# Optimization experiments

Hardware: AMD Instinct MI355X
Metric: run time of the kernel (lower is better)

## Reference

```python
import jax, jax.numpy as jnp
import numpy as np

B, L, D, H = 4, 2048, 512, 8
HD = D // H
NEG = -1e9


def setup_inputs() -> dict:
    key = jax.random.key(0)
    ks = jax.random.split(key, 11)
    s = 1.0 / np.sqrt(D)
    inp = {
        "q": jax.random.normal(ks[0], (B, L, D), jnp.float32),
        "k": jax.random.normal(ks[1], (B, L, D), jnp.float32),
        "v": jax.random.normal(ks[2], (B, L, D), jnp.float32),
        "mask": jnp.broadcast_to(jnp.tril(jnp.ones((L, L), jnp.int32)), (B, L, L)),
        "Wq": jax.random.normal(ks[3], (D, D), jnp.float32) * s,
        "bq": jax.random.normal(ks[4], (D,), jnp.float32) * s,
        "Wk": jax.random.normal(ks[5], (D, D), jnp.float32) * s,
        "bk": jax.random.normal(ks[6], (D,), jnp.float32) * s,
        "Wv": jax.random.normal(ks[7], (D, D), jnp.float32) * s,
        "bv": jax.random.normal(ks[8], (D,), jnp.float32) * s,
        "Wo": jax.random.normal(ks[9], (D, D), jnp.float32) * s,
        "bo": jax.random.normal(ks[10], (D,), jnp.float32) * s,
    }
    return inp


def reference(q, k, v, mask, Wq, bq, Wk, bk, Wv, bv, Wo, bo):
    # Linear projections (torch Linear: x @ W.T + b)
    Q = (q @ Wq.T + bq).reshape(B, L, H, HD).transpose(0, 2, 1, 3)  # [B,H,L,hd]
    K = (k @ Wk.T + bk).reshape(B, L, H, HD).transpose(0, 2, 1, 3)
    V = (v @ Wv.T + bv).reshape(B, L, H, HD).transpose(0, 2, 1, 3)
    # scaled dot-product attention with masked_fill(mask==0, -1e9)
    score = jnp.einsum('bhqd,bhkd->bhqk', Q, K) / jnp.sqrt(jnp.float32(HD))
    score = jnp.where(mask[:, None, :, :] == 0, NEG, score)
    attn = jax.nn.softmax(score, axis=-1)
    ctx = jnp.einsum('bhqk,bhkd->bhqd', attn, V)  # [B,H,L,hd]
    ctx = ctx.transpose(0, 2, 1, 3).reshape(B, L, D)
    return ctx @ Wo.T + bo
```

## Files before the change

### kernel.cpp

```cpp
#include <hip/hip_runtime.h>
#include <hip/hip_bf16.h>
#include <math.h>

constexpr int Bc  = 4;
constexpr int Lc  = 2048;
constexpr int Dc  = 512;
constexpr int Hc  = 8;
constexpr int HDc = 64;

constexpr int GK = Dc;
constexpr int BK = 64;

typedef __attribute__((ext_vector_type(8))) short bf16x8;
typedef __attribute__((ext_vector_type(4))) short bf16x4;
typedef __attribute__((ext_vector_type(4))) float f32x4;
typedef __attribute__((ext_vector_type(16))) float f32x16;
typedef __attribute__((ext_vector_type(4))) int i32x4;

static __device__ __forceinline__ short f2bf(float x) {
    __hip_bfloat16 h = __float2bfloat16(x);
    return (short)__builtin_bit_cast(unsigned short, h);
}

static __device__ __forceinline__ int cvtpk_bf16(float lo, float hi) {
    int r;
    asm("v_cvt_pk_bf16_f32 %0, %1, %2" : "=v"(r) : "v"(lo), "v"(hi));
    return r;
}

static __device__ __forceinline__ void gload_lds16(const void* g, void* l) {
    __builtin_amdgcn_global_load_lds(
        (const __attribute__((address_space(1))) void*)g,
        (__attribute__((address_space(3))) void*)l, 16, 0, 0);
}

__global__ __launch_bounds__(256)
void cast_all(const float* __restrict__ q, const float* __restrict__ k,
              const float* __restrict__ v, const float* __restrict__ wq,
              const float* __restrict__ wk, const float* __restrict__ wv,
              const float* __restrict__ wo, short* __restrict__ dst) {
    const size_t i = ((size_t)blockIdx.x * 256 + threadIdx.x) * 8;
    const float* src; size_t off;
    if      (i <  4194304) { src = q;  off = i; }
    else if (i <  8388608) { src = k;  off = i -  4194304; }
    else if (i < 12582912) { src = v;  off = i -  8388608; }
    else if (i < 12845056) { src = wq; off = i - 12582912; }
    else if (i < 13107200) { src = wk; off = i - 12845056; }
    else if (i < 13369344) { src = wv; off = i - 13107200; }
    else                   { src = wo; off = i - 13369344; }
    const float4 a = *(const float4*)(src + off);
    const float4 b = *(const float4*)(src + off + 4);
    bf16x8 o;
    o[0] = f2bf(a.x); o[1] = f2bf(a.y); o[2] = f2bf(a.z); o[3] = f2bf(a.w);
    o[4] = f2bf(b.x); o[5] = f2bf(b.y); o[6] = f2bf(b.z); o[7] = f2bf(b.w);
    *(bf16x8*)(dst + i) = o;
}

template<int BM, int BN, int WMT, int WNT>
__device__ __forceinline__ void gemm_tile(const short* __restrict__ A,
                                          const short* __restrict__ W,
                                          short* As, short* Bs,
                                          f32x4 (&acc)[WMT][WNT],
                                          int m0, int n0) {
    const int tid  = threadIdx.x;
    const int w    = tid >> 6;
    const int lane = tid & 63;
    const int low4 = lane & 15;
    const int quad = lane >> 4;
    const int wm   = w & 1, wn = w >> 1;
    const int lrow = lane >> 3;
    const int lchk = (lane & 7) * 8;

    for (int k0 = 0; k0 < GK; k0 += BK) {
#pragma unroll
        for (int i = 0; i < BM / 32; ++i) {
            const int r0 = i * 32 + w * 8;
            gload_lds16(A + (size_t)(m0 + r0 + lrow) * GK + k0 + lchk, As + r0 * BK);
        }
#pragma unroll
        for (int i = 0; i < BN / 32; ++i) {
            const int r0 = i * 32 + w * 8;
            gload_lds16(W + (size_t)(n0 + r0 + lrow) * GK + k0 + lchk, Bs + r0 * BK);
        }
        __syncthreads();
#pragma unroll
        for (int ks = 0; ks < 2; ++ks) {
            bf16x8 af[WMT], bfr[WNT];
#pragma unroll
            for (int mi = 0; mi < WMT; ++mi)
                af[mi] = *(const bf16x8*)(As + (wm * WMT * 16 + mi * 16 + low4) * BK + ks * 32 + quad * 8);
#pragma unroll
            for (int ni = 0; ni < WNT; ++ni)
                bfr[ni] = *(const bf16x8*)(Bs + (wn * WNT * 16 + ni * 16 + low4) * BK + ks * 32 + quad * 8);
#pragma unroll
            for (int mi = 0; mi < WMT; ++mi)
#pragma unroll
                for (int ni = 0; ni < WNT; ++ni)
                    acc[mi][ni] = __builtin_amdgcn_mfma_f32_16x16x32_bf16(af[mi], bfr[ni], acc[mi][ni], 0, 0, 0);
        }
        __syncthreads();
    }
}

__global__ __launch_bounds__(256)
void qkv_gemm(const short* __restrict__ Xq, const short* __restrict__ Xk,
              const short* __restrict__ Xv, const short* __restrict__ Wcat,
              const float* __restrict__ bq, const float* __restrict__ bk,
              const float* __restrict__ bv,
              short* __restrict__ Qw, short* __restrict__ Kw, short* __restrict__ Vw) {
    __shared__ __align__(16) short Smem[128 * 138];
    short* As = Smem;
    short* Bs = Smem + 8192;
    short* Ts = Smem;

    const int tid = threadIdx.x;
    const int i    = blockIdx.x;
    const int slot = i >> 3;
    const int g    = (i & 7) + 8 * (slot >> 2);
    const int j    = slot & 3;
    const int z    = g >> 6;
    const int m0   = (g & 63) * 128;
    const int n0   = z * 512 + j * 128;

    const short* A    = (z == 0) ? Xq : (z == 1) ? Xk : Xv;
    const float* bias = (z == 0) ? bq : (z == 1) ? bk : bv;

    f32x4 acc[4][4];
#pragma unroll
    for (int mi = 0; mi < 4; ++mi)
#pragma unroll
        for (int ni = 0; ni < 4; ++ni) acc[mi][ni] = (f32x4){0.f, 0.f, 0.f, 0.f};

    gemm_tile<128, 128, 4, 4>(A, Wcat, As, Bs, acc, m0, n0);

    const int lane = tid & 63, w = tid >> 6;
    const int low4 = lane & 15, quad = lane >> 4;
    const int wm = w & 1, wn = w >> 1;

    if (z < 2) {
        short* Y = (z == 0) ? Qw : Kw;
#pragma unroll
        for (int mi = 0; mi < 4; ++mi)
#pragma unroll
            for (int ni = 0; ni < 4; ++ni)
#pragma unroll
                for (int r = 0; r < 4; ++r) {
                    const int rowL = wm * 64 + mi * 16 + quad * 4 + r;
                    const int colL = wn * 64 + ni * 16 + low4;
                    const int c    = (n0 & 511) + colL;
                    Ts[rowL * 138 + colL] = f2bf(acc[mi][ni][r] + bias[c]);
                }
        __syncthreads();
        const int jj = tid & 7;
        const int b = m0 >> 11;
#pragma unroll
        for (int it = 0; it < 8; ++it) {
            const int slot2 = it * 32 + (tid >> 3);
            const int row  = slot2 >> 1, half = slot2 & 1;
            const int c0 = (n0 & 511) + half * 64;
            const int h  = c0 >> 6;
            const int l  = (m0 & 2047) + row;
            short* dst = Y + (((size_t)b * Hc + h) * Lc + l) * HDc + jj * 8;
            *(bf16x8*)dst = *(const bf16x8*)(Ts + row * 138 + half * 64 + jj * 8);
        }
    } else {
#pragma unroll
        for (int mi = 0; mi < 4; ++mi)
#pragma unroll
            for (int ni = 0; ni < 4; ++ni)
#pragma unroll
                for (int r = 0; r < 4; ++r) {
                    const int rowL = wm * 64 + mi * 16 + quad * 4 + r;
                    const int colL = wn * 64 + ni * 16 + low4;
                    const int c    = (n0 + colL) & 511;
                    Ts[colL * 136 + rowL] = f2bf(acc[mi][ni][r] + bias[c]);
                }
        __syncthreads();
        const int hdl = tid >> 1, seg = tid & 1;
        const int c  = (n0 + hdl) & 511;
        const int h  = c >> 6, hd = c & 63;
        const int b  = m0 >> 11, l0 = (m0 & 2047) + seg * 64;
        short* dst = Vw + (((size_t)b * Hc + h) * HDc + hd) * Lc + l0;
        const short* srcT = Ts + hdl * 136 + seg * 64;
#pragma unroll
        for (int jj = 0; jj < 8; ++jj)
            *(bf16x8*)(dst + jj * 8) = *(const bf16x8*)(srcT + jj * 8);
    }
}

__global__ __launch_bounds__(256)
void out_gemm(const short* __restrict__ A, const short* __restrict__ W,
              const float* __restrict__ bias, float* __restrict__ Y) {
    __shared__ __align__(16) float SmemF[64 * 132];
    short* As = (short*)SmemF;
    short* Bs = As + 64 * BK;
    float* Tf = SmemF;

    const int tid = threadIdx.x;
    const int i    = blockIdx.x;
    const int slot = i >> 3;
    const int g    = (i & 7) + 8 * (slot >> 2);
    const int j    = slot & 3;
    const int m0   = g * 64;
    const int n0   = j * 128;

    f32x4 acc[2][4];
#pragma unroll
    for (int mi = 0; mi < 2; ++mi)
#pragma unroll
        for (int ni = 0; ni < 4; ++ni) acc[mi][ni] = (f32x4){0.f, 0.f, 0.f, 0.f};

    gemm_tile<64, 128, 2, 4>(A, W, As, Bs, acc, m0, n0);

    const int lane = tid & 63, w = tid >> 6;
    const int low4 = lane & 15, quad = lane >> 4;
    const int wm = w & 1, wn = w >> 1;
#pragma unroll
    for (int mi = 0; mi < 2; ++mi)
#pragma unroll
        for (int ni = 0; ni < 4; ++ni)
#pragma unroll
            for (int r = 0; r < 4; ++r) {
                const int rowL = wm * 32 + mi * 16 + quad * 4 + r;
                const int colL = wn * 64 + ni * 16 + low4;
                Tf[rowL * 132 + colL] = acc[mi][ni][r] + bias[n0 + colL];
            }
    __syncthreads();

    const int c = (tid & 31) * 4;
#pragma unroll
    for (int p = 0; p < 8; ++p) {
        const int row = p * 8 + (tid >> 5);
        *(float4*)(Y + (size_t)(m0 + row) * Dc + n0 + c) =
            *(const float4*)(Tf + row * 132 + c);
    }
}

__global__ __launch_bounds__(256, 2)
void flash_attn(const short* __restrict__ Qb, const short* __restrict__ Kb,
                const short* __restrict__ VTb, short* __restrict__ ctx) {
    __shared__ __align__(16) short Kf[3][4096];
    __shared__ __align__(16) short Vf[3][4096];

    const int tid  = threadIdx.x;
    const int w    = tid >> 6;
    const int lane = tid & 63;
    const int t31  = lane & 31;
    const int hh   = lane >> 5;
    const int x7   = t31 & 7;

    const int u  = blockIdx.x;
    const int bh = u & 31;
    const int m  = (u < 256) ? (u >> 5) : (15 - ((u - 256) >> 5));
    const int nt = 2 * m + 2;
    const int q0w = m * 128 + w * 32;

    const short* Qg = Qb  + (size_t)bh * Lc * HDc;
    const short* Kg = Kb  + (size_t)bh * Lc * HDc;
    const short* Vg = VTb + (size_t)bh * HDc * Lc;

    bf16x8 qa[4];
#pragma unroll
    for (int hc = 0; hc < 4; ++hc)
        qa[hc] = *(const bf16x8*)(Qg + (size_t)(q0w + t31) * HDc + hc * 16 + hh * 8);
#pragma unroll
    for (int hc = 0; hc < 4; ++hc)
        asm volatile("" :: "v"(qa[hc]));

    const int grow = lane >> 3;
    const int gcol = ((lane & 7) ^ grow) * 8;

#define STAGE(KT_, BUF_)                                                       \
    {                                                                          \
        _Pragma("unroll")                                                      \
        for (int p = 0; p < 2; ++p) {                                          \
            const int ii = w + 4 * p;                                          \
            gload_lds16(Kg + (size_t)((KT_) + ii * 8 + grow) * HDc + gcol,     \
                        &Kf[BUF_][ii * 512]);                                  \
            gload_lds16(Vg + (size_t)(ii * 8 + grow) * Lc + (KT_) + gcol,      \
                        &Vf[BUF_][ii * 512]);                                  \
        }                                                                      \
    }

    STAGE(0, 0);
    STAGE(64, 1);
    asm volatile("s_waitcnt vmcnt(4)" ::: "memory");
    __builtin_amdgcn_sched_barrier(0);
    __builtin_amdgcn_s_barrier();

    f32x16 o0, o1;
#pragma unroll
    for (int i = 0; i < 16; ++i) { o0[i] = 0.f; o1[i] = 0.f; }
    float lps = 0.f;

    const float C8 = 0.18033688f;
    int br = 0;

    for (int t = 0; t < nt; ++t) {
        const int kt = t * 64;
        const int bs = (br + 2 >= 3) ? br - 1 : br + 2;
        if (t + 2 < nt) STAGE(kt + 128, bs);

        if (kt <= q0w + 31) {
            f32x16 s0, s1;
#pragma unroll
            for (int i = 0; i < 16; ++i) { s0[i] = 0.f; s1[i] = 0.f; }
            const short* kfb = Kf[br];
#pragma unroll
            for (int hc = 0; hc < 4; ++hc) {
                const int cb = ((hc * 2 + hh) ^ x7) << 3;
                const bf16x8 k0 = *(const bf16x8*)(kfb + t31 * 64 + cb);
                const bf16x8 k1 = *(const bf16x8*)(kfb + (32 + t31) * 64 + cb);
                s0 = __builtin_amdgcn_mfma_f32_32x32x16_bf16(k0, qa[hc], s0, 0, 0, 0);
                s1 = __builtin_amdgcn_mfma_f32_32x32x16_bf16(k1, qa[hc], s1, 0, 0, 0);
            }

            if (kt + 63 <= q0w) {
#pragma unroll
                for (int r = 0; r < 16; ++r) {
                    const float p0 = exp2f(s0[r] * C8);
                    const float p1 = exp2f(s1[r] * C8);
                    lps += p0 + p1; s0[r] = p0; s1[r] = p1;
                }
            } else {
                const int qv = q0w + t31;
                const int kb0 = kt + 4 * hh;
#pragma unroll
                for (int r = 0; r < 16; ++r) {
                    const int kl = kb0 + (r & 3) + 8 * (r >> 2);
                    const float p0 = (kl      <= qv) ? exp2f(s0[r] * C8) : 0.f;
                    const float p1 = (kl + 32 <= qv) ? exp2f(s1[r] * C8) : 0.f;
                    lps += p0 + p1; s0[r] = p0; s1[r] = p1;
                }
            }

            const short* vfb = Vf[br];
#pragma unroll
            for (int kc = 0; kc < 4; ++kc) {
                const int g = 8 * (kc & 1);
                float e0, e1, e2, e3, e4, e5, e6, e7;
                if (kc < 2) { e0=s0[g]; e1=s0[g+1]; e2=s0[g+2]; e3=s0[g+3];
                              e4=s0[g+4]; e5=s0[g+5]; e6=s0[g+6]; e7=s0[g+7]; }
                else        { e0=s1[g]; e1=s1[g+1]; e2=s1[g+2]; e3=s1[g+3];
                              e4=s1[g+4]; e5=s1[g+5]; e6=s1[g+6]; e7=s1[g+7]; }
                int u0 = cvtpk_bf16(e0, e1);
                int u1 = cvtpk_bf16(e2, e3);
                int v0 = cvtpk_bf16(e4, e5);
                int v1 = cvtpk_bf16(e6, e7);
                asm volatile("v_permlane32_swap_b32 %0, %1" : "+v"(u0), "+v"(v0));
                asm volatile("v_permlane32_swap_b32 %0, %1" : "+v"(u1), "+v"(v1));
                i32x4 pw; pw[0] = u0; pw[1] = u1; pw[2] = v0; pw[3] = v1;
                const bf16x8 pa = __builtin_bit_cast(bf16x8, pw);

                const int cb = ((kc * 2 + hh) ^ x7) << 3;
                const bf16x8 vf0 = *(const bf16x8*)(vfb + t31 * 64 + cb);
                const bf16x8 vf1 = *(const bf16x8*)(vfb + (32 + t31) * 64 + cb);
                o0 = __builtin_amdgcn_mfma_f32_32x32x16_bf16(pa, vf0, o0, 0, 0, 0);
                o1 = __builtin_amdgcn_mfma_f32_32x32x16_bf16(pa, vf1, o1, 0, 0, 0);
            }
        }

        if (t + 2 < nt) asm volatile("s_waitcnt vmcnt(4)" ::: "memory");
        else            asm volatile("s_waitcnt vmcnt(0)" ::: "memory");
        __builtin_amdgcn_sched_barrier(0);
        __builtin_amdgcn_s_barrier();
        br = (br + 1 >= 3) ? 0 : br + 1;
    }

    lps += __shfl_xor(lps, 32, 64);
    const float inv = 1.f / lps;
    const int b = bh >> 3, head = bh & 7;
    short* cg = ctx + (size_t)b * Lc * Dc + (size_t)head * HDc;
#pragma unroll
    for (int r = 0; r < 16; ++r) {
        const int qloc = (r & 3) + 8 * (r >> 2) + 4 * hh;
        const float iq = __shfl(inv, qloc, 64);
        short* row = cg + (size_t)(q0w + qloc) * Dc;
        row[t31]      = f2bf(o0[r] * iq);
        row[32 + t31] = f2bf(o1[r] * iq);
    }
#undef STAGE
}

extern "C" void kernel_launch(void* const* d_in, const int* in_sizes, int n_in,
                              void* d_out, int out_size, void* d_ws, size_t ws_size,
                              hipStream_t stream) {
    const float* q  = (const float*)d_in[0];
    const float* k  = (const float*)d_in[1];
    const float* v  = (const float*)d_in[2];
    const float* Wq = (const float*)d_in[4];
    const float* bq = (const float*)d_in[5];
    const float* Wk = (const float*)d_in[6];
    const float* bk = (const float*)d_in[7];
    const float* Wv = (const float*)d_in[8];
    const float* bv = (const float*)d_in[9];
    const float* Wo = (const float*)d_in[10];
    const float* bo = (const float*)d_in[11];
    float* out = (float*)d_out;

    const size_t per = (size_t)Bc * Lc * Dc;
    const size_t wsz = (size_t)Dc * Dc;
    short* Xq   = (short*)d_ws;
    short* Xk   = Xq + per;
    short* Xv   = Xk + per;
    short* Wcat = Xv + per;
    short* Wob  = Wcat + 3 * wsz;
    short* Qw   = Wob + wsz;
    short* Kw   = Qw + per;
    short* Vw   = Kw + per;
    short* Cw   = Vw + per;

    cast_all<<<6656, 256, 0, stream>>>(q, k, v, Wq, Wk, Wv, Wo, Xq);

    qkv_gemm<<<768, 256, 0, stream>>>(Xq, Xk, Xv, Wcat,
                                      bq, bk, bv, Qw, Kw, Vw);

    flash_attn<<<512, 256, 0, stream>>>(Qw, Kw, Vw, Cw);

    out_gemm<<<512, 256, 0, stream>>>(Cw, Wob, bo, out);
}
```

Before: 238.0 us.

## Split attention keys across waves and pair causal query tiles per block

The flash attention kernel now processes two 64-query parts per block, row-blocks a and 31-a, so every block gets the same causal workload. Within a part, the four waves split the work as two query columns by two key halves. Each key tile is therefore processed by half the waves, and only the diagonal tile needs masking. Partial outputs and row sums from the second key half are combined through shared memory before normalization and the store. The cost is more K/V tile staging per query overall, extra barriers and an LDS reduction per part, and larger shared-memory use that may reduce occupancy.

```diff
diff --git a/kernel.cpp b/kernel.cpp
--- a/kernel.cpp
+++ b/kernel.cpp
@@ -241,6 +241,8 @@
                 const short* __restrict__ VTb, short* __restrict__ ctx) {
     __shared__ __align__(16) short Kf[3][4096];
     __shared__ __align__(16) short Vf[3][4096];
+    __shared__ __align__(16) float Cb[2][64 * 36];
+    __shared__ float Cl[2][64];
 
     const int tid  = threadIdx.x;
     const int w    = tid >> 6;
@@ -248,27 +250,23 @@
     const int t31  = lane & 31;
     const int hh   = lane >> 5;
     const int x7   = t31 & 7;
+    const int qcol = w & 1;
+    const int kh   = w >> 1;
 
     const int u  = blockIdx.x;
     const int bh = u & 31;
-    const int m  = (u < 256) ? (u >> 5) : (15 - ((u - 256) >> 5));
-    const int nt = 2 * m + 2;
-    const int q0w = m * 128 + w * 32;
+    const int pm = u >> 5;
 
     const short* Qg = Qb  + (size_t)bh * Lc * HDc;
     const short* Kg = Kb  + (size_t)bh * Lc * HDc;
     const short* Vg = VTb + (size_t)bh * HDc * Lc;
 
-    bf16x8 qa[4];
-#pragma unroll
-    for (int hc = 0; hc < 4; ++hc)
-        qa[hc] = *(const bf16x8*)(Qg + (size_t)(q0w + t31) * HDc + hc * 16 + hh * 8);
-#pragma unroll
-    for (int hc = 0; hc < 4; ++hc)
-        asm volatile("" :: "v"(qa[hc]));
-
     const int grow = lane >> 3;
     const int gcol = ((lane & 7) ^ grow) * 8;
+
+    const float C8 = 0.18033688f;
+    const int bb = bh >> 3, head = bh & 7;
+    short* cg = ctx + (size_t)bb * Lc * Dc + (size_t)head * HDc;
 
 #define STAGE(KT_, BUF_)                                                       \
     {                                                                          \
@@ -282,103 +280,133 @@
         }                                                                      \
     }
 
-    STAGE(0, 0);
-    STAGE(64, 1);
-    asm volatile("s_waitcnt vmcnt(4)" ::: "memory");
-    __builtin_amdgcn_sched_barrier(0);
-    __builtin_amdgcn_s_barrier();
-
-    f32x16 o0, o1;
-#pragma unroll
-    for (int i = 0; i < 16; ++i) { o0[i] = 0.f; o1[i] = 0.f; }
-    float lps = 0.f;
-
-    const float C8 = 0.18033688f;
-    int br = 0;
-
-    for (int t = 0; t < nt; ++t) {
-        const int kt = t * 64;
-        const int bs = (br + 2 >= 3) ? br - 1 : br + 2;
-        if (t + 2 < nt) STAGE(kt + 128, bs);
-
-        if (kt <= q0w + 31) {
-            f32x16 s0, s1;
-#pragma unroll
-            for (int i = 0; i < 16; ++i) { s0[i] = 0.f; s1[i] = 0.f; }
-            const short* kfb = Kf[br];
-#pragma unroll
-            for (int hc = 0; hc < 4; ++hc) {
-                const int cb = ((hc * 2 + hh) ^ x7) << 3;
-                const bf16x8 k0 = *(const bf16x8*)(kfb + t31 * 64 + cb);
-                const bf16x8 k1 = *(const bf16x8*)(kfb + (32 + t31) * 64 + cb);
-                s0 = __builtin_amdgcn_mfma_f32_32x32x16_bf16(k0, qa[hc], s0, 0, 0, 0);
-                s1 = __builtin_amdgcn_mfma_f32_32x32x16_bf16(k1, qa[hc], s1, 0, 0, 0);
-            }
-
-            if (kt + 63 <= q0w) {
-#pragma unroll
-                for (int r = 0; r < 16; ++r) {
-                    const float p0 = exp2f(s0[r] * C8);
-                    const float p1 = exp2f(s1[r] * C8);
-                    lps += p0 + p1; s0[r] = p0; s1[r] = p1;
-                }
-            } else {
-                const int qv = q0w + t31;
-                const int kb0 = kt + 4 * hh;
-#pragma unroll
-                for (int r = 0; r < 16; ++r) {
-                    const int kl = kb0 + (r & 3) + 8 * (r >> 2);
-                    const float p0 = (kl      <= qv) ? exp2f(s0[r] * C8) : 0.f;
-                    const float p1 = (kl + 32 <= qv) ? exp2f(s1[r] * C8) : 0.f;
-                    lps += p0 + p1; s0[r] = p0; s1[r] = p1;
-                }
-            }
-
-            const short* vfb = Vf[br];
-#pragma unroll
-            for (int kc = 0; kc < 4; ++kc) {
-                const int g = 8 * (kc & 1);
-                float e0, e1, e2, e3, e4, e5, e6, e7;
-                if (kc < 2) { e0=s0[g]; e1=s0[g+1]; e2=s0[g+2]; e3=s0[g+3];
-                              e4=s0[g+4]; e5=s0[g+5]; e6=s0[g+6]; e7=s0[g+7]; }
-                else        { e0=s1[g]; e1=s1[g+1]; e2=s1[g+2]; e3=s1[g+3];
-                              e4=s1[g+4]; e5=s1[g+5]; e6=s1[g+6]; e7=s1[g+7]; }
-                int u0 = cvtpk_bf16(e0, e1);
-                int u1 = cvtpk_bf16(e2, e3);
-                int v0 = cvtpk_bf16(e4, e5);
-                int v1 = cvtpk_bf16(e6, e7);
-                asm volatile("v_permlane32_swap_b32 %0, %1" : "+v"(u0), "+v"(v0));
-                asm volatile("v_permlane32_swap_b32 %0, %1" : "+v"(u1), "+v"(v1));
-                i32x4 pw; pw[0] = u0; pw[1] = u1; pw[2] = v0; pw[3] = v1;
-                const bf16x8 pa = __builtin_bit_cast(bf16x8, pw);
-
-                const int cb = ((kc * 2 + hh) ^ x7) << 3;
-                const bf16x8 vf0 = *(const bf16x8*)(vfb + t31 * 64 + cb);
-                const bf16x8 vf1 = *(const bf16x8*)(vfb + (32 + t31) * 64 + cb);
-                o0 = __builtin_amdgcn_mfma_f32_32x32x16_bf16(pa, vf0, o0, 0, 0, 0);
-                o1 = __builtin_amdgcn_mfma_f32_32x32x16_bf16(pa, vf1, o1, 0, 0, 0);
-            }
-        }
-
-        if (t + 2 < nt) asm volatile("s_waitcnt vmcnt(4)" ::: "memory");
-        else            asm volatile("s_waitcnt vmcnt(0)" ::: "memory");
+    auto run_part = [&](int a) {
+        const int n  = a + 1;
+        const int q0 = a * 64 + qcol * 32;
+
+        bf16x8 qa[4];
+#pragma unroll
+        for (int hc = 0; hc < 4; ++hc)
+            qa[hc] = *(const bf16x8*)(Qg + (size_t)(q0 + t31) * HDc + hc * 16 + hh * 8);
+
+        STAGE(0, 0);
+        if (n > 1) {
+            STAGE(64, 1);
+            asm volatile("s_waitcnt vmcnt(4)" ::: "memory");
+        } else {
+            asm volatile("s_waitcnt vmcnt(0)" ::: "memory");
+        }
         __builtin_amdgcn_sched_barrier(0);
         __builtin_amdgcn_s_barrier();
-        br = (br + 1 >= 3) ? 0 : br + 1;
-    }
-
-    lps += __shfl_xor(lps, 32, 64);
-    const float inv = 1.f / lps;
-    const int b = bh >> 3, head = bh & 7;
-    short* cg = ctx + (size_t)b * Lc * Dc + (size_t)head * HDc;
-#pragma unroll
-    for (int r = 0; r < 16; ++r) {
-        const int qloc = (r & 3) + 8 * (r >> 2) + 4 * hh;
-        const float iq = __shfl(inv, qloc, 64);
-        short* row = cg + (size_t)(q0w + qloc) * Dc;
-        row[t31]      = f2bf(o0[r] * iq);
-        row[32 + t31] = f2bf(o1[r] * iq);
-    }
+
+        f32x16 o0, o1;
+#pragma unroll
+        for (int i = 0; i < 16; ++i) { o0[i] = 0.f; o1[i] = 0.f; }
+        float lps = 0.f;
+        int br = 0;
+
+        for (int t = 0; t < n; ++t) {
+            const int bs = (br + 2 >= 3) ? br - 1 : br + 2;
+            if (t + 2 < n) STAGE((t + 2) * 64, bs);
+
+            const bool lastT = (t == a);
+            if (!(lastT && qcol == 0 && kh == 1)) {
+                f32x16 s;
+#pragma unroll
+                for (int i = 0; i < 16; ++i) s[i] = 0.f;
+                const short* kfb = Kf[br];
+#pragma unroll
+                for (int hc = 0; hc < 4; ++hc) {
+                    const int cb = ((hc * 2 + hh) ^ x7) << 3;
+                    const bf16x8 kfr = *(const bf16x8*)(kfb + (kh * 32 + t31) * 64 + cb);
+                    s = __builtin_amdgcn_mfma_f32_32x32x16_bf16(kfr, qa[hc], s, 0, 0, 0);
+                }
+
+                if (lastT && !(qcol == 1 && kh == 0)) {
+                    const int qv  = q0 + t31;
+                    const int kb0 = t * 64 + kh * 32 + 4 * hh;
+#pragma unroll
+                    for (int r = 0; r < 16; ++r) {
+                        const int kl = kb0 + (r & 3) + 8 * (r >> 2);
+                        const float p = (kl <= qv) ? exp2f(s[r] * C8) : 0.f;
+                        lps += p; s[r] = p;
+                    }
+                } else {
+#pragma unroll
+                    for (int r = 0; r < 16; ++r) {
+                        const float p = exp2f(s[r] * C8);
+                        lps += p; s[r] = p;
+                    }
+                }
+
+                const short* vfb = Vf[br];
+#pragma unroll
+                for (int kc = 0; kc < 2; ++kc) {
+                    const int g = 8 * kc;
+                    int u0 = cvtpk_bf16(s[g],     s[g + 1]);
+                    int u1 = cvtpk_bf16(s[g + 2], s[g + 3]);
+                    int v0 = cvtpk_bf16(s[g + 4], s[g + 5]);
+                    int v1 = cvtpk_bf16(s[g + 6], s[g + 7]);
+                    asm volatile("v_permlane32_swap_b32 %0, %1" : "+v"(u0), "+v"(v0));
+                    asm volatile("v_permlane32_swap_b32 %0, %1" : "+v"(u1), "+v"(v1));
+                    i32x4 pw; pw[0] = u0; pw[1] = u1; pw[2] = v0; pw[3] = v1;
+                    const bf16x8 pa = __builtin_bit_cast(bf16x8, pw);
+
+                    const int cbv = ((kh * 4 + kc * 2 + hh) ^ x7) << 3;
+                    const bf16x8 vf0 = *(const bf16x8*)(vfb + t31 * 64 + cbv);
+                    const bf16x8 vf1 = *(const bf16x8*)(vfb + (32 + t31) * 64 + cbv);
+                    o0 = __builtin_amdgcn_mfma_f32_32x32x16_bf16(pa, vf0, o0, 0, 0, 0);
+                    o1 = __builtin_amdgcn_mfma_f32_32x32x16_bf16(pa, vf1, o1, 0, 0, 0);
+                }
+            }
+
+            if (t + 2 < n) asm volatile("s_waitcnt vmcnt(4)" ::: "memory");
+            else           asm volatile("s_waitcnt vmcnt(0)" ::: "memory");
+            __builtin_amdgcn_sched_barrier(0);
+            __builtin_amdgcn_s_barrier();
+            br = (br + 1 >= 3) ? 0 : br + 1;
+        }
+
+        lps += __shfl_xor(lps, 32, 64);
+
+        if (kh == 1) {
+#pragma unroll
+            for (int j = 0; j < 4; ++j) {
+                f32x4 a0 = {o0[4 * j], o0[4 * j + 1], o0[4 * j + 2], o0[4 * j + 3]};
+                f32x4 a1 = {o1[4 * j], o1[4 * j + 1], o1[4 * j + 2], o1[4 * j + 3]};
+                *(f32x4*)&Cb[qcol][lane * 36 + j * 4]      = a0;
+                *(f32x4*)&Cb[qcol][lane * 36 + 16 + j * 4] = a1;
+            }
+            Cl[qcol][lane] = lps;
+        }
+        __syncthreads();
+        if (kh == 0) {
+            lps += Cl[qcol][lane];
+#pragma unroll
+            for (int j = 0; j < 4; ++j) {
+                const f32x4 a0 = *(const f32x4*)&Cb[qcol][lane * 36 + j * 4];
+                const f32x4 a1 = *(const f32x4*)&Cb[qcol][lane * 36 + 16 + j * 4];
+#pragma unroll
+                for (int e = 0; e < 4; ++e) {
+                    o0[4 * j + e] += a0[e];
+                    o1[4 * j + e] += a1[e];
+                }
+            }
+            const float inv = 1.f / lps;
+#pragma unroll
+            for (int r = 0; r < 16; ++r) {
+                const int qloc = (r & 3) + 8 * (r >> 2) + 4 * hh;
+                const float iq = __shfl(inv, qloc, 64);
+                short* row = cg + (size_t)(q0 - qcol * 32 + qcol * 32 + qloc) * Dc;
+                row[t31]      = f2bf(o0[r] * iq);
+                row[32 + t31] = f2bf(o1[r] * iq);
+            }
+        }
+        __syncthreads();
+    };
+
+    run_part(31 - pm);
+    run_part(pm);
 #undef STAGE
 }
 
```

New measurement: 228.0 us. -4.2%, faster.
